# Optimization experiments

Measured on AMD Instinct MI355X. Metric: run time of the kernel, lower is better.

The kernel has to match this reference:

```python
import jax, jax.numpy as jnp
import numpy as np

# Dims (match init_kwargs / input_specs)
B, S, HID = 1, 2048, 2048
NH, NKV, HD = 16, 4, 128          # head_dim = HID // NH
REP = NH // NKV                    # num_key_value_groups
BLOCK_SIZE, LOCAL_BLOCKS, SINK_NUM = 8, 4, 4
SCALING = HD ** -0.5


def rotate_half(x):
    x1, x2 = jnp.split(x, 2, axis=-1)
    return jnp.concatenate([-x2, x1], axis=-1)


def setup_inputs() -> dict:
    key = jax.random.key(0)
    ks = jax.random.split(key, 7)
    return {
        "hidden_states": jax.random.normal(ks[0], (B, S, HID), jnp.float32),
        "cos": jax.random.uniform(ks[1], (B, S, HD), jnp.float32, minval=-1.0, maxval=1.0),
        "sin": jax.random.uniform(ks[2], (B, S, HD), jnp.float32, minval=-1.0, maxval=1.0),
        # Projection weights stored as [in, out] so x @ W matches nn.Linear (bias=False).
        "Wq": 0.02 * jax.random.normal(ks[3], (HID, NH * HD), jnp.float32),
        "Wk": 0.02 * jax.random.normal(ks[4], (HID, NKV * HD), jnp.float32),
        "Wv": 0.02 * jax.random.normal(ks[5], (HID, NKV * HD), jnp.float32),
        "Wo": 0.02 * jax.random.normal(ks[6], (NH * HD, HID), jnp.float32),
    }


def sink_local_mask(seq_len):
    # query i attends to: sink tokens j < min(SINK_NUM, i), and local window
    # max(0, i - LOCAL_BLOCKS*BLOCK_SIZE) <= j <= i (diagonal included so every
    # row has at least one valid key; see notes).
    i = jnp.arange(seq_len)[:, None]
    j = jnp.arange(seq_len)[None, :]
    sink = j < jnp.minimum(SINK_NUM, i)
    local = (j >= i - LOCAL_BLOCKS * BLOCK_SIZE) & (j <= i)
    return sink | local  # [S, S] bool, broadcast over (B, H)


def reference(hidden_states, cos, sin, Wq, Wk, Wv, Wo):
    # projections -> [B, H, S, D]
    q = (hidden_states @ Wq).reshape(B, S, NH, HD).transpose(0, 2, 1, 3)
    k = (hidden_states @ Wk).reshape(B, S, NKV, HD).transpose(0, 2, 1, 3)
    v = (hidden_states @ Wv).reshape(B, S, NKV, HD).transpose(0, 2, 1, 3)
    # rotary embedding, cos/sin broadcast over head dim (unsqueeze_dim=1)
    c = cos[:, None, :, :]
    s = sin[:, None, :, :]
    q = q * c + rotate_half(q) * s
    k = k * c + rotate_half(k) * s
    # repeat_kv (GQA) -> [B, NH, S, D]
    k = jnp.repeat(k, REP, axis=1)
    v = jnp.repeat(v, REP, axis=1)
    # sink + local sparse attention (dense compute + mask, as in source)
    scores = jnp.einsum('bhqd,bhkd->bhqk', q, k) * SCALING
    mask = sink_local_mask(S)
    scores = jnp.where(mask, scores, -jnp.inf)
    attn_weights = jax.nn.softmax(scores, axis=-1)
    attn_output = jnp.einsum('bhqk,bhkd->bhqd', attn_weights, v)
    # Faithful to source: view(B, S, -1) on the [B, H, S, D] layout WITHOUT a
    # transpose(1,2) first (the original code omits it).
    attn_output = attn_output.reshape(B, S, NH * HD)
    attn_output = attn_output @ Wo
    return attn_output, attn_weights
```

## Files before the change

### kernel.cpp

```cpp
#include <hip/hip_runtime.h>

typedef unsigned short ushort_t;
typedef __attribute__((ext_vector_type(8))) short short8;
typedef __attribute__((ext_vector_type(4))) float f32x4;
typedef __attribute__((ext_vector_type(8))) unsigned short us8;
typedef __attribute__((ext_vector_type(4))) unsigned short us4;

#define SEQ 2048
#define HIDD 2048
#define XLD 3072
#define SCALING 0.08838834764831843f

__device__ __forceinline__ float bf2f(ushort_t u) {
    unsigned int x = ((unsigned int)u) << 16;
    return __builtin_bit_cast(float, x);
}
__device__ __forceinline__ ushort_t f2bf(float f) {
    unsigned int u = __builtin_bit_cast(unsigned int, f);
    u += 0x7fffu + ((u >> 16) & 1u);
    return (ushort_t)(u >> 16);
}

__device__ __forceinline__ void transpose_tile(
    const float* __restrict__ W, ushort_t* __restrict__ Wt,
    int N, int n0, int k0, int dstRow0) {
    __shared__ ushort_t t[64 * 80];
    const int tid = threadIdx.x;
    {
        const int kl = tid >> 4;
        const int nc = (tid & 15) * 4;
        #pragma unroll
        for (int p = 0; p < 4; ++p) {
            int k = kl + p * 16;
            float4 v = *(const float4*)(W + (size_t)(k0 + k) * N + n0 + nc);
            t[(nc + 0) * 80 + k] = f2bf(v.x);
            t[(nc + 1) * 80 + k] = f2bf(v.y);
            t[(nc + 2) * 80 + k] = f2bf(v.z);
            t[(nc + 3) * 80 + k] = f2bf(v.w);
        }
    }
    __syncthreads();
    {
        const int nl = tid >> 3;
        const int kc = (tid & 7) * 8;
        #pragma unroll
        for (int p = 0; p < 2; ++p) {
            int n = nl + p * 32;
            *(us8*)(Wt + (size_t)(dstRow0 + n) * HIDD + k0 + kc) =
                *(const us8*)&t[n * 80 + kc];
        }
    }
}

__global__ __launch_bounds__(256) void transpose_all(
    const float* __restrict__ Wq, const float* __restrict__ Wk,
    const float* __restrict__ Wv, const float* __restrict__ Wo,
    const float* __restrict__ hid,
    ushort_t* __restrict__ Wqkvt, ushort_t* __restrict__ Wot,
    ushort_t* __restrict__ Hb) {
    int bx = blockIdx.x, k0 = blockIdx.y * 64;
    if (bx < 32)       transpose_tile(Wq, Wqkvt, 2048, bx * 64,        k0, bx * 64);
    else if (bx < 40)  transpose_tile(Wk, Wqkvt, 512,  (bx - 32) * 64, k0, 2048 + (bx - 32) * 64);
    else if (bx < 48)  transpose_tile(Wv, Wqkvt, 512,  (bx - 40) * 64, k0, 2560 + (bx - 40) * 64);
    else if (bx < 80)  transpose_tile(Wo, Wot,   2048, (bx - 48) * 64, k0, (bx - 48) * 64);
    else {
        int chunk = (bx - 80) * 32 + blockIdx.y;
        size_t base = (size_t)chunk * 4096 + threadIdx.x * 16;
        #pragma unroll
        for (int p = 0; p < 4; ++p) {
            float4 v = *(const float4*)(hid + base + p * 4);
            us4 o;
            o[0] = f2bf(v.x); o[1] = f2bf(v.y); o[2] = f2bf(v.z); o[3] = f2bf(v.w);
            *(us4*)(Hb + base + p * 4) = o;
        }
    }
}

__global__ __launch_bounds__(256) void gemm_splitk(
    const ushort_t* __restrict__ A, int lda,
    const ushort_t* __restrict__ Bt, int ldb,
    ushort_t* __restrict__ P, int ldc,
    const int4 kexts) {
    __shared__ ushort_t lA[2 * 128 * 32];
    __shared__ ushort_t lB[2 * 128 * 32];
    const int tid = threadIdx.x;
    const int wave = tid >> 6, lane = tid & 63;
    const int wm = wave >> 1, wn = wave & 1;
    const int quad = lane >> 4, l16 = lane & 15;
    const int m0 = blockIdx.y * 128, n0 = blockIdx.x * 128;
    const int z = blockIdx.z;

    const int ke[4] = {kexts.x, kexts.y, kexts.z, kexts.w};
    int koff = 0;
    for (int zz = 0; zz < 4; ++zz) if (zz < z) koff += ke[zz];
    const int kext = ke[z];

    A  += (size_t)koff;
    Bt += (size_t)koff;
    P  += (size_t)z * ((size_t)gridDim.y * 128) * ldc;

    const int srow = lane >> 2;
    const int scol = 8 * ((lane & 3) ^ (srow & 3));

    f32x4 acc[4][4] = {};

    const ushort_t* Ab = A  + (size_t)(m0 + wave * 16 + srow) * lda + scol;
    const ushort_t* Bb = Bt + (size_t)(n0 + wave * 16 + srow) * ldb + scol;
    ushort_t* lAw = lA + (wave * 16) * 32;
    ushort_t* lBw = lB + (wave * 16) * 32;

    const int rsw = (quad ^ (l16 & 3)) * 8;

    for (int kk = 0; kk < kext; kk += 64) {
        __syncthreads();
        #pragma unroll
        for (int kh = 0; kh < 2; ++kh) {
            #pragma unroll
            for (int c = 0; c < 2; ++c) {
                __builtin_amdgcn_global_load_lds(
                    (const __attribute__((address_space(1))) unsigned int*)(const void*)
                        (Ab + (size_t)(c * 64) * lda + kk + kh * 32),
                    (__attribute__((address_space(3))) unsigned int*)(void*)
                        (lAw + kh * 128 * 32 + c * 64 * 32), 16, 0, 0);
                __builtin_amdgcn_global_load_lds(
                    (const __attribute__((address_space(1))) unsigned int*)(const void*)
                        (Bb + (size_t)(c * 64) * ldb + kk + kh * 32),
                    (__attribute__((address_space(3))) unsigned int*)(void*)
                        (lBw + kh * 128 * 32 + c * 64 * 32), 16, 0, 0);
            }
        }
        __syncthreads();
        #pragma unroll
        for (int kh = 0; kh < 2; ++kh) {
            short8 af[4], bfr[4];
            #pragma unroll
            for (int mt = 0; mt < 4; ++mt)
                af[mt] = *(const short8*)&lA[kh * 128 * 32 + (wm * 64 + mt * 16 + l16) * 32 + rsw];
            #pragma unroll
            for (int nt = 0; nt < 4; ++nt)
                bfr[nt] = *(const short8*)&lB[kh * 128 * 32 + (wn * 64 + nt * 16 + l16) * 32 + rsw];
            #pragma unroll
            for (int mt = 0; mt < 4; ++mt) {
                #pragma unroll
                for (int nt = 0; nt < 4; ++nt)
                    acc[mt][nt] = __builtin_amdgcn_mfma_f32_16x16x32_bf16(
                        af[mt], bfr[nt], acc[mt][nt], 0, 0, 0);
            }
        }
    }

    #pragma unroll
    for (int mt = 0; mt < 4; ++mt) {
        #pragma unroll
        for (int nt = 0; nt < 4; ++nt) {
            int gm = m0 + wm * 64 + mt * 16 + quad * 4;
            int gn = n0 + wn * 64 + nt * 16 + l16;
            #pragma unroll
            for (int r = 0; r < 4; ++r)
                P[(size_t)(gm + r) * ldc + gn] = f2bf(acc[mt][nt][r]);
        }
    }
}

#define ROPE_THREADS (SEQ * 20 * 64)
__global__ __launch_bounds__(256) void reduce_x(
    const ushort_t* __restrict__ P, ushort_t* __restrict__ X,
    const float* __restrict__ cosp, const float* __restrict__ sinp) {
    const size_t ZS = (size_t)SEQ * XLD;
    int idx = blockIdx.x * 256 + threadIdx.x;
    if (idx < ROPE_THREADS) {
        int d = idx & 63;
        int rem = idx >> 6;
        int hh = rem % 20;
        int s = rem / 20;
        int cb = (hh < 16) ? hh * 128 : 2048 + (hh - 16) * 128;
        size_t base = (size_t)s * XLD + cb;
        float x1 = bf2f(P[base + d])      + bf2f(P[ZS + base + d]);
        float x2 = bf2f(P[base + d + 64]) + bf2f(P[ZS + base + d + 64]);
        const float* cr = cosp + (size_t)s * 128;
        const float* sr = sinp + (size_t)s * 128;
        X[base + d]      = f2bf(x1 * cr[d]      - x2 * sr[d]);
        X[base + d + 64] = f2bf(x2 * cr[d + 64] + x1 * sr[d + 64]);
    } else {
        int v = (idx - ROPE_THREADS) * 4;
        int c = v & 511;
        int s = v >> 9;
        size_t base = (size_t)s * XLD + 2560 + c;
        us4 a = *(const us4*)(P + base);
        us4 b = *(const us4*)(P + ZS + base);
        us4 o;
        #pragma unroll
        for (int t = 0; t < 4; ++t) o[t] = f2bf(bf2f(a[t]) + bf2f(b[t]));
        *(us4*)(X + base) = o;
    }
}

__global__ __launch_bounds__(256) void reduce_out3(
    const ushort_t* __restrict__ P, float* __restrict__ out) {
    const size_t ZS = (size_t)SEQ * HIDD;
    size_t idx = ((size_t)blockIdx.x * 256 + threadIdx.x) * 4;
    us4 a = *(const us4*)(P + idx);
    us4 b = *(const us4*)(P + ZS + idx);
    us4 c = *(const us4*)(P + 2 * ZS + idx);
    float4 o;
    o.x = bf2f(a[0]) + bf2f(b[0]) + bf2f(c[0]);
    o.y = bf2f(a[1]) + bf2f(b[1]) + bf2f(c[1]);
    o.z = bf2f(a[2]) + bf2f(b[2]) + bf2f(c[2]);
    o.w = bf2f(a[3]) + bf2f(b[3]) + bf2f(c[3]);
    *(float4*)(out + idx) = o;
}

__global__ __launch_bounds__(256) void attn_kernel(
    const ushort_t* __restrict__ X, float* __restrict__ Wts,
    ushort_t* __restrict__ Aout) {
    int g = blockIdx.x * 4 + (threadIdx.x >> 6);
    int lane = threadIdx.x & 63;
    int i = g & (SEQ - 1);
    int h = g >> 11;

    const ushort_t* Q = X + (size_t)i * XLD + h * 128;
    unsigned int qv = *(const unsigned int*)(Q + 2 * lane);
    float q0 = bf2f((ushort_t)(qv & 0xffff));
    float q1 = bf2f((ushort_t)(qv >> 16));

    int lo = i - 32; if (lo < 0) lo = 0;
    int nsink = lo < 4 ? lo : 4;
    int NJ = nsink + (i - lo + 1);

    const ushort_t* Kbase = X + 2048 + (h >> 2) * 128;
    const ushort_t* Vbase = X + 2560 + (h >> 2) * 128;

    float m = -1e30f, mysc = -1e30f;
    for (int jj = 0; jj < NJ; ++jj) {
        int j = (jj < nsink) ? jj : (lo + jj - nsink);
        unsigned int kv = *(const unsigned int*)(Kbase + (size_t)j * XLD + 2 * lane);
        float p = q0 * bf2f((ushort_t)(kv & 0xffff)) + q1 * bf2f((ushort_t)(kv >> 16));
        #pragma unroll
        for (int off = 32; off > 0; off >>= 1) p += __shfl_xor(p, off, 64);
        p *= SCALING;
        if (jj == lane) mysc = p;
        m = fmaxf(m, p);
    }
    float e = (lane < NJ) ? expf(mysc - m) : 0.f;
    float l = e;
    #pragma unroll
    for (int off = 32; off > 0; off >>= 1) l += __shfl_xor(l, off, 64);
    float w = e / l;

    float* row = Wts + ((size_t)h * SEQ + i) * SEQ;
    #pragma unroll
    for (int s = 0; s < 8; ++s) {
        float4 o;
        #pragma unroll
        for (int t = 0; t < 4; ++t) {
            int c = s * 256 + lane * 4 + t;
            bool in = (c < nsink) || (c >= lo && c <= i);
            int jjc = in ? ((c < nsink) ? c : (nsink + c - lo)) : 0;
            float wv = __shfl(w, jjc, 64);
            o[t] = in ? wv : 0.f;
        }
        *(float4*)(row + s * 256 + lane * 4) = o;
    }

    float o0 = 0.f, o1 = 0.f;
    for (int jj = 0; jj < NJ; ++jj) {
        int j = (jj < nsink) ? jj : (lo + jj - nsink);
        float pb = __shfl(w, jj, 64);
        unsigned int vv = *(const unsigned int*)(Vbase + (size_t)j * XLD + 2 * lane);
        o0 += pb * bf2f((ushort_t)(vv & 0xffff));
        o1 += pb * bf2f((ushort_t)(vv >> 16));
    }
    int r = h * 128 + (i >> 4);
    int c = (i & 15) * 128 + 2 * lane;
    ushort_t* Ar = Aout + (size_t)r * HIDD + c;
    Ar[0] = f2bf(o0);
    Ar[1] = f2bf(o1);
}

extern "C" void kernel_launch(void* const* d_in, const int* in_sizes, int n_in,
                              void* d_out, int out_size, void* d_ws, size_t ws_size,
                              hipStream_t stream) {
    if (n_in < 7) return;
    const float* hid  = (const float*)d_in[0];
    const float* cosp = (const float*)d_in[1];
    const float* sinp = (const float*)d_in[2];
    const float* Wq   = (const float*)d_in[3];
    const float* Wk   = (const float*)d_in[4];
    const float* Wv   = (const float*)d_in[5];
    const float* Wo   = (const float*)d_in[6];

    float* out = (float*)d_out;
    float* wts = out + (size_t)SEQ * HIDD;

    ushort_t* Hb    = (ushort_t*)d_ws;
    ushort_t* Wqkvt = Hb    + (size_t)2048 * 2048;
    ushort_t* Wot   = Wqkvt + (size_t)3072 * 2048;
    ushort_t* X     = Wot   + (size_t)2048 * 2048;
    ushort_t* Am    = X     + (size_t)SEQ * XLD;
    ushort_t* Pqkv  = Am    + (size_t)SEQ * HIDD;
    ushort_t* Pout  = Pqkv  + 2 * (size_t)SEQ * XLD;
    size_t need = ((char*)(Pout + 3 * (size_t)SEQ * HIDD)) - (char*)d_ws;
    if (ws_size < need) return;

    dim3 blk(256);
    transpose_all<<<dim3(112, 32), blk, 0, stream>>>(
        Wq, Wk, Wv, Wo, hid, Wqkvt, Wot, Hb);

    gemm_splitk<<<dim3(24, 16, 2), blk, 0, stream>>>(
        Hb, HIDD, Wqkvt, 2048, Pqkv, XLD, make_int4(1024, 1024, 0, 0));
    reduce_x<<<(ROPE_THREADS + SEQ * 512 / 4) / 256, blk, 0, stream>>>(
        Pqkv, X, cosp, sinp);

    attn_kernel<<<(SEQ * 16) / 4, blk, 0, stream>>>(X, wts, Am);

    gemm_splitk<<<dim3(16, 16, 3), blk, 0, stream>>>(
        Am, HIDD, Wot, 2048, Pout, HIDD, make_int4(704, 704, 640, 0));
    reduce_out3<<<(SEQ * HIDD) / (256 * 4), blk, 0, stream>>>(Pout, out);
}
```

Measured before the change: 521.7 us.

## Overlap dense attention-weight expansion with output projection GEMM in one kernel

The attention kernel now writes only the compact per-row softmax weights (up to 37 values) to a workspace instead of expanding each 2048-wide fp32 row. A new fused kernel interleaves the Wo split-k GEMM blocks with blocks that expand those compact weights into the dense 256 MB weight tensor using nontemporal stores. The intent is to overlap the bandwidth-bound mask write with compute-bound GEMM work. The cost is an extra small workspace round trip, and expansion blocks keep the GEMM's shared-memory footprint, which can lower occupancy.

Result: slower. 585.7 us (+12.3%).

```diff
diff --git a/kernel.cpp b/kernel.cpp
--- a/kernel.cpp
+++ b/kernel.cpp
@@ -76,19 +76,16 @@
     }
 }
 
-__global__ __launch_bounds__(256) void gemm_splitk(
+__device__ __forceinline__ void gemm_body(
     const ushort_t* __restrict__ A, int lda,
     const ushort_t* __restrict__ Bt, int ldb,
     ushort_t* __restrict__ P, int ldc,
-    const int4 kexts) {
-    __shared__ ushort_t lA[2 * 128 * 32];
-    __shared__ ushort_t lB[2 * 128 * 32];
+    int m0, int n0, int z, const int4 kexts, int zstride,
+    ushort_t* lA, ushort_t* lB) {
     const int tid = threadIdx.x;
     const int wave = tid >> 6, lane = tid & 63;
     const int wm = wave >> 1, wn = wave & 1;
     const int quad = lane >> 4, l16 = lane & 15;
-    const int m0 = blockIdx.y * 128, n0 = blockIdx.x * 128;
-    const int z = blockIdx.z;
 
     const int ke[4] = {kexts.x, kexts.y, kexts.z, kexts.w};
     int koff = 0;
@@ -97,7 +94,7 @@
 
     A  += (size_t)koff;
     Bt += (size_t)koff;
-    P  += (size_t)z * ((size_t)gridDim.y * 128) * ldc;
+    P  += (size_t)z * (size_t)zstride * ldc;
 
     const int srow = lane >> 2;
     const int scol = 8 * ((lane & 3) ^ (srow & 3));
@@ -158,6 +155,58 @@
             #pragma unroll
             for (int r = 0; r < 4; ++r)
                 P[(size_t)(gm + r) * ldc + gn] = f2bf(acc[mt][nt][r]);
+        }
+    }
+}
+
+__global__ __launch_bounds__(256) void gemm_qkv(
+    const ushort_t* __restrict__ A, const ushort_t* __restrict__ Bt,
+    ushort_t* __restrict__ P) {
+    __shared__ ushort_t lA[2 * 128 * 32];
+    __shared__ ushort_t lB[2 * 128 * 32];
+    gemm_body(A, HIDD, Bt, HIDD, P, XLD,
+              blockIdx.y * 128, blockIdx.x * 128, blockIdx.z,
+              make_int4(1024, 1024, 0, 0), SEQ, lA, lB);
+}
+
+__global__ __launch_bounds__(256) void wo_expand(
+    const ushort_t* __restrict__ Am, const ushort_t* __restrict__ Wot,
+    ushort_t* __restrict__ P,
+    const float* __restrict__ cw, float* __restrict__ wts) {
+    __shared__ ushort_t lA[2 * 128 * 32];
+    __shared__ ushort_t lB[2 * 128 * 32];
+    int bx = blockIdx.x;
+    if ((bx & 3) != 3) {
+        int g = bx - ((bx + 1) >> 2);
+        int z = g >> 8, rem = g & 255;
+        gemm_body(Am, HIDD, Wot, HIDD, P, HIDD,
+                  (rem >> 4) * 128, (rem & 15) * 128, z,
+                  make_int4(704, 704, 640, 0), SEQ, lA, lB);
+    } else {
+        int e = bx >> 2;
+        int wave = threadIdx.x >> 6, lane = threadIdx.x & 63;
+        int row0 = e * 128 + wave * 32;
+        for (int r = 0; r < 32; ++r) {
+            int row = row0 + r;
+            int i = row & (SEQ - 1);
+            int lo = i - 32; if (lo < 0) lo = 0;
+            int nsink = lo < 4 ? lo : 4;
+            int NJ = nsink + (i - lo + 1);
+            float wv = (lane < NJ) ? cw[(size_t)row * 40 + lane] : 0.f;
+            float* orow = wts + (size_t)row * SEQ;
+            #pragma unroll
+            for (int s = 0; s < 8; ++s) {
+                f32x4 o;
+                #pragma unroll
+                for (int t = 0; t < 4; ++t) {
+                    int c = s * 256 + lane * 4 + t;
+                    bool in = (c < nsink) || (c >= lo && c <= i);
+                    int jjc = in ? ((c < nsink) ? c : (nsink + c - lo)) : 0;
+                    float val = __shfl(wv, jjc, 64);
+                    o[t] = in ? val : 0.f;
+                }
+                __builtin_nontemporal_store(o, (f32x4*)(orow + s * 256 + lane * 4));
+            }
         }
     }
 }
@@ -211,7 +260,7 @@
 }
 
 __global__ __launch_bounds__(256) void attn_kernel(
-    const ushort_t* __restrict__ X, float* __restrict__ Wts,
+    const ushort_t* __restrict__ X, float* __restrict__ cw,
     ushort_t* __restrict__ Aout) {
     int g = blockIdx.x * 4 + (threadIdx.x >> 6);
     int lane = threadIdx.x & 63;
@@ -247,20 +296,7 @@
     for (int off = 32; off > 0; off >>= 1) l += __shfl_xor(l, off, 64);
     float w = e / l;
 
-    float* row = Wts + ((size_t)h * SEQ + i) * SEQ;
-    #pragma unroll
-    for (int s = 0; s < 8; ++s) {
-        float4 o;
-        #pragma unroll
-        for (int t = 0; t < 4; ++t) {
-            int c = s * 256 + lane * 4 + t;
-            bool in = (c < nsink) || (c >= lo && c <= i);
-            int jjc = in ? ((c < nsink) ? c : (nsink + c - lo)) : 0;
-            float wv = __shfl(w, jjc, 64);
-            o[t] = in ? wv : 0.f;
-        }
-        *(float4*)(row + s * 256 + lane * 4) = o;
-    }
+    if (lane < NJ) cw[(size_t)g * 40 + lane] = w;
 
     float o0 = 0.f, o1 = 0.f;
     for (int jj = 0; jj < NJ; ++jj) {
@@ -299,21 +335,20 @@
     ushort_t* Am    = X     + (size_t)SEQ * XLD;
     ushort_t* Pqkv  = Am    + (size_t)SEQ * HIDD;
     ushort_t* Pout  = Pqkv  + 2 * (size_t)SEQ * XLD;
-    size_t need = ((char*)(Pout + 3 * (size_t)SEQ * HIDD)) - (char*)d_ws;
+    float*    cw    = (float*)(Pout + 3 * (size_t)SEQ * HIDD);
+    size_t need = ((char*)(cw + (size_t)32768 * 40)) - (char*)d_ws;
     if (ws_size < need) return;
 
     dim3 blk(256);
     transpose_all<<<dim3(112, 32), blk, 0, stream>>>(
         Wq, Wk, Wv, Wo, hid, Wqkvt, Wot, Hb);
 
-    gemm_splitk<<<dim3(24, 16, 2), blk, 0, stream>>>(
-        Hb, HIDD, Wqkvt, 2048, Pqkv, XLD, make_int4(1024, 1024, 0, 0));
+    gemm_qkv<<<dim3(24, 16, 2), blk, 0, stream>>>(Hb, Wqkvt, Pqkv);
     reduce_x<<<(ROPE_THREADS + SEQ * 512 / 4) / 256, blk, 0, stream>>>(
         Pqkv, X, cosp, sinp);
 
-    attn_kernel<<<(SEQ * 16) / 4, blk, 0, stream>>>(X, wts, Am);
-
-    gemm_splitk<<<dim3(16, 16, 3), blk, 0, stream>>>(
-        Am, HIDD, Wot, 2048, Pout, HIDD, make_int4(704, 704, 640, 0));
+    attn_kernel<<<(SEQ * 16) / 4, blk, 0, stream>>>(X, cw, Am);
+
+    wo_expand<<<dim3(1024), blk, 0, stream>>>(Am, Wot, Pout, cw, wts);
     reduce_out3<<<(SEQ * HIDD) / (256 * 4), blk, 0, stream>>>(Pout, out);
 }
```
